# Kernel tuning notes

Measured on AMD Instinct MI355X. Metric: run time of the kernel, lower is better.

The kernel has to match this reference:

```python
import jax, jax.numpy as jnp
import numpy as np

D_STATE = 16
D_CONV = 4


def _ln_cf(x, w, b, eps=1e-6):
    # channels_first LayerNorm over dim 1 of (B,C,H,W)
    u = x.mean(1, keepdims=True)
    s = ((x - u) ** 2).mean(1, keepdims=True)
    return w[:, None, None] * ((x - u) / jnp.sqrt(s + eps)) + b[:, None, None]


def _ln_last(x, w, b, eps=1e-5):
    u = x.mean(-1, keepdims=True)
    s = ((x - u) ** 2).mean(-1, keepdims=True)
    return (x - u) / jnp.sqrt(s + eps) * w + b


def _mamba(xn, Win, convw, convb, Wx, Wdt, bdt, Alog, Dp):
    # xn: (B, L, d_model); returns (B, L, d_inner) (out_proj is Identity in this module)
    B, L, _ = xn.shape
    di = Win.shape[0] // 2
    xz = xn @ Win.T                                   # (B,L,2*di), in_proj bias=False
    xc, z = xz[..., :di], xz[..., di:]
    # causal depthwise conv1d along L (pad left d_conv-1, slice == torch pad+trim)
    xt = jnp.pad(xc.transpose(0, 2, 1), ((0, 0), (0, 0), (D_CONV - 1, 0)))
    xt = jax.lax.conv_general_dilated(xt, convw[:, None, :], (1,), 'VALID',
                                      dimension_numbers=('NCH', 'OIH', 'NCH'),
                                      feature_group_count=di)
    xs = jax.nn.silu(xt + convb[None, :, None]).transpose(0, 2, 1)  # (B,L,di)
    dtr = Wdt.shape[1]
    x_dbl = xs @ Wx.T                                 # (B,L,dtr+2*ds)
    dt = x_dbl[..., :dtr]
    Bm = x_dbl[..., dtr:dtr + D_STATE]                # (B,L,ds)
    Cm = x_dbl[..., dtr + D_STATE:]                   # (B,L,ds)
    delta = jax.nn.softplus(dt @ Wdt.T + bdt)         # (B,L,di)
    A = -jnp.exp(Alog)                                # (di,ds)
    dA = jnp.exp(delta[..., None] * A)                # (B,L,di,ds)
    dBx = delta[..., None] * Bm[:, :, None, :] * xs[..., None]

    def step(h, ab):
        a, b2 = ab
        h = a * h + b2
        return h, h

    h0 = jnp.zeros((B, di, D_STATE), xn.dtype)
    _, hs = jax.lax.scan(step, h0, (dA.transpose(1, 0, 2, 3), dBx.transpose(1, 0, 2, 3)))
    y = jnp.einsum('lbds,bls->bld', hs, Cm) + xs * Dp
    return y * jax.nn.silu(z)


def _dwconv2d(u, k, dil):
    c = k.shape[0]
    return jax.lax.conv_general_dilated(u, k[:, None], (1, 1),
                                        [(dil, dil), (dil, dil)],
                                        rhs_dilation=(dil, dil),
                                        dimension_numbers=('NCHW', 'OIHW', 'NCHW'),
                                        feature_group_count=c)


def _block(x, gamma1, gamma2, ln1_w, ln1_b, mn_w, mn_b,
           f_Win, f_convw, f_convb, f_Wx, f_Wdt, f_bdt, f_Alog, f_D,
           b_Win, b_convw, b_convb, b_Wx, b_Wdt, b_bdt, b_Alog, b_D,
           Wout, msff_win, msff_dw1, msff_dw2, msff_dw3, msff_wout):
    B, C, H, W = x.shape
    L = H * W
    # --- BiPixelMambaLayer branch ---
    x1 = _ln_cf(x, ln1_w, ln1_b)                       # norm1 (channels_first)
    xf = x1.reshape(B, C, L).transpose(0, 2, 1)        # (B,L,C)
    xn = _ln_last(xf, mn_w, mn_b)                      # inner nn.LayerNorm (eps=1e-5)
    yf = _mamba(xn, f_Win, f_convw, f_convb, f_Wx, f_Wdt, f_bdt, f_Alog, f_D)
    yb = _mamba(xn[:, ::-1], b_Win, b_convw, b_convb, b_Wx, b_Wdt, b_bdt, b_Alog, b_D)
    yo = (yf + yb[:, ::-1]) @ Wout.T                   # shared out_proj (bias=False)
    x = x + gamma1[:, None, None] * (yo.transpose(0, 2, 1).reshape(B, C, H, W) + x1)
    # --- MSFF branch (norm1 reused) ---
    inp = x
    xm = _ln_cf(x, ln1_w, ln1_b)
    h = jnp.einsum('oc,bchw->bohw', msff_win, xm)      # project_in (1x1x1 conv, depth=1)
    hid = msff_dw1.shape[0]
    h1 = _dwconv2d(h[:, :hid], msff_dw1, 1)            # Conv3d 3x3x3 w/ depth=1 == 2D center slice
    h2 = _dwconv2d(h[:, hid:2 * hid], msff_dw2, 2)
    h3 = _dwconv2d(h[:, 2 * hid:], msff_dw3, 3)
    g = jax.nn.gelu(h1, approximate=False) * h2 * h3
    xm = jnp.einsum('oc,bchw->bohw', msff_wout, g)     # project_out
    return inp + gamma2[:, None, None] * xm


def setup_inputs() -> dict:
    key = jax.random.key(0)
    ks = jax.random.split(key, 40)
    dim, di, dtr, ds, hid, Bn, H, W = 96, 192, 6, 16, 192, 2, 64, 64
    r = lambda i, shape, s=0.05: jax.random.normal(ks[i], shape, jnp.float32) * s
    inp = {
        'x': r(0, (Bn, dim, H, W), 1.0),
        'gamma1': r(1, (dim,), 0.1), 'gamma2': r(2, (dim,), 0.1),
        'ln1_w': 1.0 + r(3, (dim,), 0.1), 'ln1_b': r(4, (dim,), 0.1),
        'mn_w': 1.0 + r(5, (dim,), 0.1), 'mn_b': r(6, (dim,), 0.1),
    }
    i = 7
    for p in ('f_', 'b_'):
        inp[p + 'Win'] = r(i, (2 * di, dim)); i += 1
        inp[p + 'convw'] = r(i, (di, D_CONV), 0.2); i += 1
        inp[p + 'convb'] = r(i, (di,), 0.1); i += 1
        inp[p + 'Wx'] = r(i, (dtr + 2 * ds, di)); i += 1
        inp[p + 'Wdt'] = r(i, (di, dtr), 0.1); i += 1
        inp[p + 'bdt'] = r(i, (di,), 0.1); i += 1
        inp[p + 'Alog'] = jax.random.uniform(ks[i], (di, ds), jnp.float32, 0.0, 2.5); i += 1
        inp[p + 'D'] = r(i, (di,), 0.5); i += 1
    inp['Wout'] = r(i, (dim, di)); i += 1
    inp['msff_win'] = r(i, (3 * hid, dim)); i += 1
    inp['msff_dw1'] = r(i, (hid, 3, 3), 0.2); i += 1
    inp['msff_dw2'] = r(i, (hid, 3, 3), 0.2); i += 1
    inp['msff_dw3'] = r(i, (hid, 3, 3), 0.2); i += 1
    inp['msff_wout'] = r(i, (dim, hid)); i += 1
    return inp


def reference(x, gamma1, gamma2, ln1_w, ln1_b, mn_w, mn_b,
              f_Win, f_convw, f_convb, f_Wx, f_Wdt, f_bdt, f_Alog, f_D,
              b_Win, b_convw, b_convb, b_Wx, b_Wdt, b_bdt, b_Alog, b_D,
              Wout, msff_win, msff_dw1, msff_dw2, msff_dw3, msff_wout):
    return _block(x, gamma1, gamma2, ln1_w, ln1_b, mn_w, mn_b,
                  f_Win, f_convw, f_convb, f_Wx, f_Wdt, f_bdt, f_Alog, f_D,
                  b_Win, b_convw, b_convb, b_Wx, b_Wdt, b_bdt, b_Alog, b_D,
                  Wout, msff_win, msff_dw1, msff_dw2, msff_dw3, msff_wout)
```

## Files before the change

### kernel.cpp

```cpp
#include <hip/hip_runtime.h>
#include <hip/hip_bf16.h>
#include <math.h>

typedef __hip_bfloat16 bf16;
typedef _Float16 f16;
typedef f16  f16x8  __attribute__((ext_vector_type(8)));
typedef short short8 __attribute__((ext_vector_type(8)));
typedef unsigned short ushort8 __attribute__((ext_vector_type(8)));
typedef float floatx4 __attribute__((ext_vector_type(4)));

#define L_SEQ 4096
#define BATCH 2
#define DIM   96
#define DI    192
#define DS    16
#define HID   192
#define NPOS  (BATCH * L_SEQ)
#define NCH   1024
#define CHUNK 4
#define GRP   32
#define NGRP  (NCH / GRP)
#define NREC  (2 * BATCH * DI)
#define LDBL  40
#define LOG2E 1.44269504088896f
#define TP    32

__device__ __forceinline__ float silu_f(float x) { return x / (1.f + __expf(-x)); }
__device__ __forceinline__ float softplus_f(float x) {
    return fmaxf(x, 0.f) + __logf(1.f + __expf(-fabsf(x)));
}
__device__ __forceinline__ float b2f(bf16 v) { return __bfloat162float(v); }
__device__ __forceinline__ float us2f(unsigned short u) {
    union { unsigned int i; float f; } cv; cv.i = ((unsigned int)u) << 16; return cv.f;
}

__global__ void k_prep(const float* __restrict__ fWin, const float* __restrict__ bWin,
                       const float* __restrict__ fWx,  const float* __restrict__ bWx,
                       const float* __restrict__ Wout, const float* __restrict__ mwin,
                       const float* __restrict__ mwout,
                       const float* __restrict__ fAlog, const float* __restrict__ bAlog,
                       const float* __restrict__ mdw1, const float* __restrict__ mdw2,
                       const float* __restrict__ mdw3,
                       bf16* __restrict__ war, float* __restrict__ a2tab,
                       float* __restrict__ mdwt) {
    int i = blockIdx.x * blockDim.x + threadIdx.x;
    if (i < 180480) {
        float v;
        if (i < 36864)        v = fWin[i];
        else if (i < 73728)   v = bWin[i - 36864];
        else if (i < 81024)   v = fWx[i - 73728];
        else if (i < 88320)   v = bWx[i - 81024];
        else if (i < 106752)  v = Wout[i - 88320];
        else if (i < 162048)  v = mwin[i - 106752];
        else                  v = mwout[i - 162048];
        war[i] = __float2bfloat16(v);
    } else if (i < 186624) {
        int j = i - 180480;
        int dir = j / 3072, rem = j % 3072;
        const float* al = dir ? bAlog : fAlog;
        a2tab[j] = -__expf(al[rem]) * LOG2E;
    } else if (i < 191808) {
        int j = i - 186624;
        int cv = j / 1728, rem = j % 1728;
        int tap = rem / 192, c = rem % 192;
        const float* src = (cv == 0) ? mdw1 : (cv == 1) ? mdw2 : mdw3;
        mdwt[j] = src[c * 9 + tap];
    }
}

__global__ void k_ln12_t(const float* __restrict__ x,
                         const float* __restrict__ ln1w, const float* __restrict__ ln1b,
                         const float* __restrict__ mnw,  const float* __restrict__ mnb,
                         float* __restrict__ X1, bf16* __restrict__ XNbf) {
    __shared__ float xt[DIM][TP + 1];
    __shared__ float rs[8][TP], rss[8][TP];
    __shared__ float uu[TP], rr[TP];
    int p0 = blockIdx.x * TP;
    int b = p0 >> 12, l0 = p0 & (L_SEQ - 1);
    int t = threadIdx.x;
    int tg = t >> 5, li = t & 31;

    for (int idx = t; idx < DIM * TP; idx += 256) {
        int c = idx >> 5, q = idx & 31;
        xt[c][q] = x[((size_t)(b * DIM + c)) * L_SEQ + l0 + q];
    }
    __syncthreads();
    {
        float s = 0.f, ss = 0.f;
        for (int c = tg; c < DIM; c += 8) { float v = xt[c][li]; s += v; ss += v * v; }
        rs[tg][li] = s; rss[tg][li] = ss;
    }
    __syncthreads();
    if (t < TP) {
        float s = 0.f, ss = 0.f;
#pragma unroll
        for (int g = 0; g < 8; g++) { s += rs[g][t]; ss += rss[g][t]; }
        float u = s / DIM;
        uu[t] = u; rr[t] = rsqrtf(ss / DIM - u * u + 1e-6f);
    }
    __syncthreads();
    {
        float u = uu[li], r = rr[li];
        float s2 = 0.f, ss2 = 0.f;
        for (int c = tg; c < DIM; c += 8) {
            float tv = ln1w[c] * (xt[c][li] - u) * r + ln1b[c];
            X1[((size_t)(b * DIM + c)) * L_SEQ + l0 + li] = tv;
            xt[c][li] = tv;
            s2 += tv; ss2 += tv * tv;
        }
        rs[tg][li] = s2; rss[tg][li] = ss2;
    }
    __syncthreads();
    if (t < TP) {
        float s = 0.f, ss = 0.f;
#pragma unroll
        for (int g = 0; g < 8; g++) { s += rs[g][t]; ss += rss[g][t]; }
        float u = s / DIM;
        uu[t] = u; rr[t] = rsqrtf(ss / DIM - u * u + 1e-5f);
    }
    __syncthreads();
    for (int idx = t; idx < DIM * TP; idx += 256) {
        int q = idx / DIM, c = idx % DIM;
        XNbf[(size_t)(p0 + q) * DIM + c] =
            __float2bfloat16((xt[c][q] - uu[q]) * rr[q] * mnw[c] + mnb[c]);
    }
}

__global__ void mfma_nt_dir(const bf16* __restrict__ A0, const bf16* __restrict__ A1,
                            const bf16* __restrict__ W0, const bf16* __restrict__ W1,
                            void* __restrict__ C0, void* __restrict__ C1,
                            int M, int N, int K, int ldc, int pad6, int obf) {
    int z = blockIdx.z;
    const bf16* A = z ? A1 : A0;
    const bf16* W = z ? W1 : W0;
    void* C = z ? C1 : C0;
    int wave = threadIdx.x >> 6, lane = threadIdx.x & 63;
    int m0 = blockIdx.x * 64 + wave * 16;
    int n0 = blockIdx.y * 64;
    int lm = lane & 15, quad = lane >> 4;
    const short* Ap = (const short*)A + (size_t)(m0 + lm) * K + quad * 8;
    const short* Wp = (const short*)W;
    floatx4 acc[4];
#pragma unroll
    for (int t = 0; t < 4; t++) acc[t] = (floatx4){0.f, 0.f, 0.f, 0.f};
    for (int k0 = 0; k0 < K; k0 += 32) {
        short8 a = *(const short8*)(Ap + k0);
#pragma unroll
        for (int t = 0; t < 4; t++) {
            int n = n0 + t * 16 + lm;
            short8 b = (n < N) ? *(const short8*)(Wp + (size_t)n * K + k0 + quad * 8)
                               : (short8){0,0,0,0,0,0,0,0};
            acc[t] = __builtin_amdgcn_mfma_f32_16x16x32_bf16(a, b, acc[t], 0, 0, 0);
        }
    }
#pragma unroll
    for (int t = 0; t < 4; t++) {
        int n = n0 + t * 16 + lm;
        if (n < N) {
            int nn = (pad6 && n >= 6) ? n + 2 : n;
#pragma unroll
            for (int r = 0; r < 4; r++) {
                int m = m0 + quad * 4 + r;
                if (obf) ((bf16*)C)[(size_t)m * ldc + nn] = __float2bfloat16(acc[t][r]);
                else     ((float*)C)[(size_t)m * ldc + nn] = acc[t][r];
            }
        }
    }
}

__global__ void mfma_nt(const bf16* __restrict__ A, const bf16* __restrict__ W,
                        bf16* __restrict__ C, int M, int N, int K, int ldc) {
    int wave = threadIdx.x >> 6, lane = threadIdx.x & 63;
    int m0 = blockIdx.x * 64 + wave * 16;
    int n0 = blockIdx.y * 64;
    int lm = lane & 15, quad = lane >> 4;
    const short* Ap = (const short*)A + (size_t)(m0 + lm) * K + quad * 8;
    const short* Wp = (const short*)W;
    floatx4 acc[4];
#pragma unroll
    for (int t = 0; t < 4; t++) acc[t] = (floatx4){0.f, 0.f, 0.f, 0.f};
    for (int k0 = 0; k0 < K; k0 += 32) {
        short8 a = *(const short8*)(Ap + k0);
#pragma unroll
        for (int t = 0; t < 4; t++) {
            int n = n0 + t * 16 + lm;
            short8 b = (n < N) ? *(const short8*)(Wp + (size_t)n * K + k0 + quad * 8)
                               : (short8){0,0,0,0,0,0,0,0};
            acc[t] = __builtin_amdgcn_mfma_f32_16x16x32_bf16(a, b, acc[t], 0, 0, 0);
        }
    }
#pragma unroll
    for (int t = 0; t < 4; t++) {
        int n = n0 + t * 16 + lm;
        if (n < N) {
#pragma unroll
            for (int r = 0; r < 4; r++) {
                int m = m0 + quad * 4 + r;
                C[(size_t)m * ldc + n] = __float2bfloat16(acc[t][r]);
            }
        }
    }
}

__global__ void mfma_out(const bf16* __restrict__ Y1, const bf16* __restrict__ Y2,
                         const bf16* __restrict__ W, float* __restrict__ C,
                         int M, int N, int K, int ldc) {
    int wave = threadIdx.x >> 6, lane = threadIdx.x & 63;
    int m0 = blockIdx.x * 64 + wave * 16;
    int n0 = blockIdx.y * 64;
    int lm = lane & 15, quad = lane >> 4;
    const short* A1p = (const short*)Y1 + (size_t)(m0 + lm) * K + quad * 8;
    const short* A2p = (const short*)Y2 + (size_t)(m0 + lm) * K + quad * 8;
    const short* Wp  = (const short*)W;
    floatx4 acc[4];
#pragma unroll
    for (int t = 0; t < 4; t++) acc[t] = (floatx4){0.f, 0.f, 0.f, 0.f};
    for (int k0 = 0; k0 < K; k0 += 32) {
        short8 a1 = *(const short8*)(A1p + k0);
        short8 a2 = *(const short8*)(A2p + k0);
#pragma unroll
        for (int t = 0; t < 4; t++) {
            int n = n0 + t * 16 + lm;
            short8 b = (n < N) ? *(const short8*)(Wp + (size_t)n * K + k0 + quad * 8)
                               : (short8){0,0,0,0,0,0,0,0};
            acc[t] = __builtin_amdgcn_mfma_f32_16x16x32_bf16(a1, b, acc[t], 0, 0, 0);
            acc[t] = __builtin_amdgcn_mfma_f32_16x16x32_bf16(a2, b, acc[t], 0, 0, 0);
        }
    }
#pragma unroll
    for (int t = 0; t < 4; t++) {
        int n = n0 + t * 16 + lm;
        if (n < N) {
#pragma unroll
            for (int r = 0; r < 4; r++) {
                int m = m0 + quad * 4 + r;
                C[(size_t)m * ldc + n] = acc[t][r];
            }
        }
    }
}

__global__ void mfma_msffout(const bf16* __restrict__ A, const bf16* __restrict__ Bm,
                             const float* __restrict__ XMID, const float* __restrict__ gamma2,
                             float* __restrict__ out, int M, int K) {
    int wave = threadIdx.x >> 6, lane = threadIdx.x & 63;
    int m0 = blockIdx.x * 64 + wave * 16;
    int n0 = blockIdx.y * 64;
    int lm = lane & 15, quad = lane >> 4;
    int am = m0 + lm;
    bool aval = am < M;
    const short* Ap = (const short*)A + (size_t)am * K + quad * 8;
    const short* Bp = (const short*)Bm;
    floatx4 acc[4];
#pragma unroll
    for (int t = 0; t < 4; t++) acc[t] = (floatx4){0.f, 0.f, 0.f, 0.f};
    for (int k0 = 0; k0 < K; k0 += 32) {
        short8 a = aval ? *(const short8*)(Ap + k0) : (short8){0,0,0,0,0,0,0,0};
#pragma unroll
        for (int t = 0; t < 4; t++) {
            int n = n0 + t * 16 + lm;
            short8 b = *(const short8*)(Bp + (size_t)n * K + k0 + quad * 8);
            acc[t] = __builtin_amdgcn_mfma_f32_16x16x32_bf16(a, b, acc[t], 0, 0, 0);
        }
    }
#pragma unroll
    for (int t = 0; t < 4; t++) {
        int n = n0 + t * 16 + lm;
        int b = n >> 12, l = n & (L_SEQ - 1);
#pragma unroll
        for (int r = 0; r < 4; r++) {
            int m = m0 + quad * 4 + r;
            if (m < M) {
                size_t idx = ((size_t)(b * M + m)) * L_SEQ + l;
                out[idx] = XMID[idx] + gamma2[m] * acc[t][r];
            }
        }
    }
}

__global__ void k_conv_v(const bf16* __restrict__ XZF, const bf16* __restrict__ XZB,
                         const float* __restrict__ fw, const float* __restrict__ fb,
                         const float* __restrict__ bw, const float* __restrict__ bb,
                         bf16* __restrict__ XSF, bf16* __restrict__ XSB) {
    int dirb = blockIdx.y;
    int i = blockIdx.x * blockDim.x + threadIdx.x;
    int dg = i % 24;
    int p = i / 24;
    int b = p >> 12, l = p & (L_SEQ - 1);
    int d0 = dg * 8;
    const bf16* XZ = dirb ? XZB : XZF;
    const float* cw = dirb ? bw : fw;
    const float* cb = dirb ? bb : fb;

    float4 w[8];
#pragma unroll
    for (int j = 0; j < 8; j++) w[j] = *(const float4*)(cw + (d0 + j) * 4);
    float acc[8];
#pragma unroll
    for (int j = 0; j < 8; j++) acc[j] = cb[d0 + j];

#pragma unroll
    for (int k = 0; k < 4; k++) {
        int ls = dirb ? (l + 3 - k) : (l - 3 + k);
        if (ls >= 0 && ls < L_SEQ) {
            ushort8 xv = *(const ushort8*)((const unsigned short*)XZ +
                           ((size_t)(b * L_SEQ + ls)) * 384 + d0);
#pragma unroll
            for (int j = 0; j < 8; j++) {
                float wk = (k == 0) ? w[j].x : (k == 1) ? w[j].y : (k == 2) ? w[j].z : w[j].w;
                acc[j] += wk * us2f(xv[j]);
            }
        }
    }
    ushort8 ov;
#pragma unroll
    for (int j = 0; j < 8; j++) {
        bf16 t = __float2bfloat16(silu_f(acc[j]));
        ov[j] = *(unsigned short*)&t;
    }
    *(ushort8*)((unsigned short*)(dirb ? XSB : XSF) + (size_t)p * DI + d0) = ov;
}

__global__ void k_scan_p1(const float* __restrict__ DBLF, const float* __restrict__ DBLB,
                          const bf16* __restrict__ XSF,  const bf16* __restrict__ XSB,
                          const float* __restrict__ fWdt, const float* __restrict__ fbdt,
                          const float* __restrict__ bWdt, const float* __restrict__ bbdt,
                          const float* __restrict__ a2tab,
                          f16* __restrict__ P, f16* __restrict__ Q) {
    int t = blockIdx.x * blockDim.x + threadIdx.x;
    int d = t % DI;
    int g = t / DI;
    int chunk = g & (NCH - 1);
    int dirb = g >> 10;
    int b = dirb & 1, dir = dirb >> 1;

    const float* DBL = dir ? DBLB : DBLF;
    const bf16*  XS  = dir ? XSB  : XSF;
    const float* wdt = (dir ? bWdt : fWdt) + d * 6;
    float bdtv = (dir ? bbdt : fbdt)[d];

    float wd[6];
#pragma unroll
    for (int r = 0; r < 6; r++) wd[r] = wdt[r];
    const float* a2p = a2tab + (dir * DI + d) * 16;
    float A2[16], h[16];
#pragma unroll
    for (int v = 0; v < 4; v++) {
        float4 a2v = *(const float4*)(a2p + 4 * v);
        A2[4*v] = a2v.x; A2[4*v+1] = a2v.y; A2[4*v+2] = a2v.z; A2[4*v+3] = a2v.w;
    }
#pragma unroll
    for (int s = 0; s < 16; s++) h[s] = 0.f;

    int l = dir ? (L_SEQ - 1 - chunk * CHUNK) : chunk * CHUNK;
    int stp = dir ? -1 : 1;
    float sumdel = 0.f;

#pragma unroll
    for (int i = 0; i < CHUNK; i++) {
        size_t p = (size_t)b * L_SEQ + l;
        const float* row = DBL + p * LDBL;
        float dtv = bdtv;
#pragma unroll
        for (int r = 0; r < 6; r++) dtv += row[r] * wd[r];
        float del = softplus_f(dtv);
        float xs  = b2f(XS[p * DI + d]);
        const float4* bm = (const float4*)(row + 8);
        float4 B0 = bm[0], B1 = bm[1], B2 = bm[2], B3 = bm[3];
        float Bm[16] = {B0.x,B0.y,B0.z,B0.w, B1.x,B1.y,B1.z,B1.w,
                        B2.x,B2.y,B2.z,B2.w, B3.x,B3.y,B3.z,B3.w};
        float dx = del * xs;
        sumdel += del;
#pragma unroll
        for (int s = 0; s < 16; s++) {
            float dA = exp2f(del * A2[s]);
            h[s] = dA * h[s] + dx * Bm[s];
        }
        l += stp;
    }
    size_t idx = ((size_t)g * DI + d) * 16;
    f16x8 q0, q1, p0, p1;
#pragma unroll
    for (int j = 0; j < 8; j++) {
        q0[j] = (f16)h[j];
        q1[j] = (f16)h[8 + j];
        p0[j] = (f16)exp2f(A2[j] * sumdel);
        p1[j] = (f16)exp2f(A2[8 + j] * sumdel);
    }
    *(f16x8*)(Q + idx)     = q0;
    *(f16x8*)(Q + idx + 8) = q1;
    *(f16x8*)(P + idx)     = p0;
    *(f16x8*)(P + idx + 8) = p1;
}

__global__ void k_scan_p2a(const f16* __restrict__ P, const f16* __restrict__ Q,
                           float* __restrict__ Pg, float* __restrict__ Qg) {
    int t = blockIdx.x * blockDim.x + threadIdx.x;
    int s8 = t & 1;
    int d = (t >> 1) % DI;
    int rest = t / (DI * 2);
    int grp = rest % NGRP;
    int dirb = rest / NGRP;

    float Pr[8], Qr[8];
#pragma unroll
    for (int j = 0; j < 8; j++) { Pr[j] = 1.f; Qr[j] = 0.f; }

    size_t base = (((size_t)(dirb * NCH + grp * GRP)) * DI + d) * 16 + s8 * 8;
    for (int i = 0; i < GRP; i++) {
        size_t idx = base + (size_t)i * (DI * 16);
        f16x8 p8 = *(const f16x8*)(P + idx);
        f16x8 q8 = *(const f16x8*)(Q + idx);
#pragma unroll
        for (int j = 0; j < 8; j++) {
            float pv = (float)p8[j], qv = (float)q8[j];
            Qr[j] = pv * Qr[j] + qv;
            Pr[j] *= pv;
        }
    }
    size_t gidx = (((size_t)(dirb * NGRP + grp)) * DI + d) * 16 + s8 * 8;
#pragma unroll
    for (int v = 0; v < 2; v++) {
        *(float4*)(Pg + gidx + 4 * v) = make_float4(Pr[4*v], Pr[4*v+1], Pr[4*v+2], Pr[4*v+3]);
        *(float4*)(Qg + gidx + 4 * v) = make_float4(Qr[4*v], Qr[4*v+1], Qr[4*v+2], Qr[4*v+3]);
    }
}

__global__ void k_scan_p2b(const float* __restrict__ Pg, float* __restrict__ Qg) {
    int u = blockIdx.x * blockDim.x + threadIdx.x;
    int s = u & 15;
    int dd = (u >> 4) % DI;
    int dirb = u / (DI * 16);
    float runP = 1.f, runQ = 0.f;
#pragma unroll
    for (int g = 0; g < NGRP; g++) {
        size_t i = (((size_t)(dirb * NGRP + g)) * DI + dd) * 16 + s;
        float pg = Pg[i], qg = Qg[i];
        Qg[i] = runQ;
        runQ = pg * runQ + qg;
        runP *= pg;
    }
}

__global__ void k_scan_p2c(const f16* __restrict__ P, f16* __restrict__ Q,
                           const float* __restrict__ Qg) {
    int t = blockIdx.x * blockDim.x + threadIdx.x;
    int s8 = t & 1;
    int d = (t >> 1) % DI;
    int rest = t / (DI * 2);
    int grp = rest % NGRP;
    int dirb = rest / NGRP;

    size_t gidx = (((size_t)(dirb * NGRP + grp)) * DI + d) * 16 + s8 * 8;
    float runQ[8];
#pragma unroll
    for (int v = 0; v < 2; v++) {
        float4 qv = *(const float4*)(Qg + gidx + 4 * v);
        runQ[4*v] = qv.x; runQ[4*v+1] = qv.y; runQ[4*v+2] = qv.z; runQ[4*v+3] = qv.w;
    }

    size_t base = (((size_t)(dirb * NCH + grp * GRP)) * DI + d) * 16 + s8 * 8;
    for (int i = 0; i < GRP; i++) {
        size_t idx = base + (size_t)i * (DI * 16);
        f16x8 p8 = *(const f16x8*)(P + idx);
        f16x8 q8 = *(const f16x8*)(Q + idx);
        f16x8 o8;
#pragma unroll
        for (int j = 0; j < 8; j++) {
            o8[j] = (f16)runQ[j];
            runQ[j] = (float)p8[j] * runQ[j] + (float)q8[j];
        }
        *(f16x8*)(Q + idx) = o8;
    }
}

__global__ void k_scan_p3(const float* __restrict__ DBLF, const float* __restrict__ DBLB,
                          const bf16* __restrict__ XSF,  const bf16* __restrict__ XSB,
                          const bf16* __restrict__ XZF,  const bf16* __restrict__ XZB,
                          const float* __restrict__ fWdt, const float* __restrict__ fbdt,
                          const float* __restrict__ bWdt, const float* __restrict__ bbdt,
                          const float* __restrict__ a2tab,
                          const float* __restrict__ fD,    const float* __restrict__ bD,
                          const f16* __restrict__ Q,
                          bf16* __restrict__ YSF, bf16* __restrict__ YSB) {
    int t = blockIdx.x * blockDim.x + threadIdx.x;
    int d = t % DI;
    int g = t / DI;
    int chunk = g & (NCH - 1);
    int dirb = g >> 10;
    int b = dirb & 1, dir = dirb >> 1;

    const float* DBL = dir ? DBLB : DBLF;
    const bf16*  XS  = dir ? XSB  : XSF;
    const bf16*  XZ  = dir ? XZB  : XZF;
    const float* wdt = (dir ? bWdt : fWdt) + d * 6;
    float bdtv = (dir ? bbdt : fbdt)[d];
    float Dp = dir ? bD[d] : fD[d];
    bf16* Y = dir ? YSB : YSF;

    float wd[6];
#pragma unroll
    for (int r = 0; r < 6; r++) wd[r] = wdt[r];
    const float* a2p = a2tab + (dir * DI + d) * 16;
    float A2[16], h[16];
#pragma unroll
    for (int v = 0; v < 4; v++) {
        float4 a2v = *(const float4*)(a2p + 4 * v);
        A2[4*v] = a2v.x; A2[4*v+1] = a2v.y; A2[4*v+2] = a2v.z; A2[4*v+3] = a2v.w;
    }
    size_t idx = ((size_t)g * DI + d) * 16;
    f16x8 q0 = *(const f16x8*)(Q + idx);
    f16x8 q1 = *(const f16x8*)(Q + idx + 8);
#pragma unroll
    for (int j = 0; j < 8; j++) { h[j] = (float)q0[j]; h[8 + j] = (float)q1[j]; }

    int l = dir ? (L_SEQ - 1 - chunk * CHUNK) : chunk * CHUNK;
    int stp = dir ? -1 : 1;

#pragma unroll
    for (int i = 0; i < CHUNK; i++) {
        size_t p = (size_t)b * L_SEQ + l;
        const float* row = DBL + p * LDBL;
        float dtv = bdtv;
#pragma unroll
        for (int r = 0; r < 6; r++) dtv += row[r] * wd[r];
        float del = softplus_f(dtv);
        float xs  = b2f(XS[p * DI + d]);
        float z   = b2f(XZ[p * 384 + 192 + d]);
        const float4* bm = (const float4*)(row + 8);
        float4 B0 = bm[0], B1 = bm[1], B2 = bm[2], B3 = bm[3];
        float4 C0 = bm[4], C1 = bm[5], C2 = bm[6], C3 = bm[7];
        float Bm[16] = {B0.x,B0.y,B0.z,B0.w, B1.x,B1.y,B1.z,B1.w,
                        B2.x,B2.y,B2.z,B2.w, B3.x,B3.y,B3.z,B3.w};
        float Cm[16] = {C0.x,C0.y,C0.z,C0.w, C1.x,C1.y,C1.z,C1.w,
                        C2.x,C2.y,C2.z,C2.w, C3.x,C3.y,C3.z,C3.w};
        float dx = del * xs;
        float pr = 0.f;
#pragma unroll
        for (int s = 0; s < 16; s++) {
            float dA = exp2f(del * A2[s]);
            h[s] = dA * h[s] + dx * Bm[s];
            pr += h[s] * Cm[s];
        }
        Y[p * DI + d] = __float2bfloat16((pr + xs * Dp) * silu_f(z));
        l += stp;
    }
}

__global__ void k_mid_t(const float* __restrict__ x, const float* __restrict__ YO,
                        const float* __restrict__ X1,
                        const float* __restrict__ gamma1,
                        const float* __restrict__ ln1w, const float* __restrict__ ln1b,
                        float* __restrict__ XMID, bf16* __restrict__ XM2cl) {
    __shared__ float vt[DIM][TP + 1];
    __shared__ float yt[DIM][TP + 1];
    __shared__ float rs[8][TP], rss[8][TP];
    __shared__ float uu[TP], rr[TP];
    int p0 = blockIdx.x * TP;
    int b = p0 >> 12, l0 = p0 & (L_SEQ - 1);
    int t = threadIdx.x;
    int tg = t >> 5, li = t & 31;

    for (int idx = t; idx < DIM * TP; idx += 256) {
        int q = idx / DIM, c = idx % DIM;
        yt[c][q] = YO[(size_t)(p0 + q) * DIM + c];
    }
    __syncthreads();
    {
        float s = 0.f, ss = 0.f;
        for (int c = tg; c < DIM; c += 8) {
            size_t gi = ((size_t)(b * DIM + c)) * L_SEQ + l0 + li;
            float v = x[gi] + gamma1[c] * (yt[c][li] + X1[gi]);
            XMID[gi] = v;
            vt[c][li] = v;
            s += v; ss += v * v;
        }
        rs[tg][li] = s; rss[tg][li] = ss;
    }
    __syncthreads();
    if (t < TP) {
        float s = 0.f, ss = 0.f;
#pragma unroll
        for (int g = 0; g < 8; g++) { s += rs[g][t]; ss += rss[g][t]; }
        float u = s / DIM;
        uu[t] = u; rr[t] = rsqrtf(ss / DIM - u * u + 1e-6f);
    }
    __syncthreads();
    for (int idx = t; idx < DIM * TP; idx += 256) {
        int q = idx / DIM, c = idx % DIM;
        XM2cl[(size_t)(p0 + q) * DIM + c] =
            __float2bfloat16(ln1w[c] * (vt[c][q] - uu[q]) * rr[q] + ln1b[c]);
    }
}

__global__ void k_msff_v(const bf16* __restrict__ H, const float* __restrict__ mdwt,
                         bf16* __restrict__ G) {
    int i = blockIdx.x * blockDim.x + threadIdx.x;
    int cg = i % 24;
    int p = i / 24;
    int c0 = cg * 8;
    int b = p >> 12, l = p & (L_SEQ - 1);
    int y = l >> 6, xc = l & 63;
    float a1[8] = {}, a2[8] = {}, a3[8] = {};
    const unsigned short* Hu = (const unsigned short*)H;

#pragma unroll
    for (int ky = 0; ky < 3; ky++) {
#pragma unroll
        for (int kx = 0; kx < 3; kx++) {
            int tap = ky * 3 + kx;
            {
                int y1 = y + (ky - 1), x1 = xc + (kx - 1);
                if (y1 >= 0 && y1 < 64 && x1 >= 0 && x1 < 64) {
                    float4 w0 = *(const float4*)(mdwt + tap * 192 + c0);
                    float4 w1 = *(const float4*)(mdwt + tap * 192 + c0 + 4);
                    ushort8 hv = *(const ushort8*)(Hu +
                        ((size_t)(b * L_SEQ + y1 * 64 + x1)) * 576 + c0);
                    float wv[8] = {w0.x,w0.y,w0.z,w0.w, w1.x,w1.y,w1.z,w1.w};
#pragma unroll
                    for (int j = 0; j < 8; j++) a1[j] += wv[j] * us2f(hv[j]);
                }
            }
            {
                int y2 = y + (ky - 1) * 2, x2 = xc + (kx - 1) * 2;
                if (y2 >= 0 && y2 < 64 && x2 >= 0 && x2 < 64) {
                    float4 w0 = *(const float4*)(mdwt + (9 + tap) * 192 + c0);
                    float4 w1 = *(const float4*)(mdwt + (9 + tap) * 192 + c0 + 4);
                    ushort8 hv = *(const ushort8*)(Hu +
                        ((size_t)(b * L_SEQ + y2 * 64 + x2)) * 576 + 192 + c0);
                    float wv[8] = {w0.x,w0.y,w0.z,w0.w, w1.x,w1.y,w1.z,w1.w};
#pragma unroll
                    for (int j = 0; j < 8; j++) a2[j] += wv[j] * us2f(hv[j]);
                }
            }
            {
                int y3 = y + (ky - 1) * 3, x3 = xc + (kx - 1) * 3;
                if (y3 >= 0 && y3 < 64 && x3 >= 0 && x3 < 64) {
                    float4 w0 = *(const float4*)(mdwt + (18 + tap) * 192 + c0);
                    float4 w1 = *(const float4*)(mdwt + (18 + tap) * 192 + c0 + 4);
                    ushort8 hv = *(const ushort8*)(Hu +
                        ((size_t)(b * L_SEQ + y3 * 64 + x3)) * 576 + 384 + c0);
                    float wv[8] = {w0.x,w0.y,w0.z,w0.w, w1.x,w1.y,w1.z,w1.w};
#pragma unroll
                    for (int j = 0; j < 8; j++) a3[j] += wv[j] * us2f(hv[j]);
                }
            }
        }
    }
    ushort8 ov;
#pragma unroll
    for (int j = 0; j < 8; j++) {
        float ge = 0.5f * a1[j] * (1.f + erff(a1[j] * 0.70710678118f));
        bf16 t = __float2bfloat16(ge * a2[j] * a3[j]);
        ov[j] = *(unsigned short*)&t;
    }
    *(ushort8*)((unsigned short*)G + (size_t)p * HID + c0) = ov;
}

extern "C" void kernel_launch(void* const* d_in, const int* in_sizes, int n_in,
                              void* d_out, int out_size, void* d_ws, size_t ws_size,
                              hipStream_t stream) {
    const float* x      = (const float*)d_in[0];
    const float* gamma1 = (const float*)d_in[1];
    const float* gamma2 = (const float*)d_in[2];
    const float* ln1w   = (const float*)d_in[3];
    const float* ln1b   = (const float*)d_in[4];
    const float* mnw    = (const float*)d_in[5];
    const float* mnb    = (const float*)d_in[6];
    const float* fWin   = (const float*)d_in[7];
    const float* fconvw = (const float*)d_in[8];
    const float* fconvb = (const float*)d_in[9];
    const float* fWx    = (const float*)d_in[10];
    const float* fWdt   = (const float*)d_in[11];
    const float* fbdt   = (const float*)d_in[12];
    const float* fAlog  = (const float*)d_in[13];
    const float* fD     = (const float*)d_in[14];
    const float* bWin   = (const float*)d_in[15];
    const float* bconvw = (const float*)d_in[16];
    const float* bconvb = (const float*)d_in[17];
    const float* bWx    = (const float*)d_in[18];
    const float* bWdt   = (const float*)d_in[19];
    const float* bbdt   = (const float*)d_in[20];
    const float* bAlog  = (const float*)d_in[21];
    const float* bD     = (const float*)d_in[22];
    const float* Wout   = (const float*)d_in[23];
    const float* mwin   = (const float*)d_in[24];
    const float* mdw1   = (const float*)d_in[25];
    const float* mdw2   = (const float*)d_in[26];
    const float* mdw3   = (const float*)d_in[27];
    const float* mwout  = (const float*)d_in[28];
    float* out = (float*)d_out;

    float* ws = (float*)d_ws;
    float* X1    = ws;
    bf16*  XNbf  = (bf16*)(ws + 786432);
    bf16*  XZF   = (bf16*)(ws + 1179648);
    bf16*  XZB   = (bf16*)(ws + 2752512);
    bf16*  XSF   = (bf16*)(ws + 4325376);
    bf16*  XSB   = (bf16*)(ws + 5111808);
    float* DBLF  = ws + 5898240;
    float* DBLB  = ws + 6225920;
    f16*   Ph    = (f16*)(ws + 6553600);
    f16*   Qh    = (f16*)(ws + 12845056);
    bf16*  YSFbf = (bf16*)(ws + 19136512);
    bf16*  YSBbf = (bf16*)(ws + 19922944);
    float* YO    = ws + 20709376;
    float* XMID  = ws + 21495808;
    bf16*  XM2cl = (bf16*)(ws + 22282240);
    bf16*  Hcl   = (bf16*)(ws + 22675456);
    bf16*  Gcl   = (bf16*)(ws + 25034752);
    bf16*  WAR   = (bf16*)(ws + 25821184);
    float* A2tab = ws + 25911424;
    float* MDWT  = ws + 25917568;
    float* Pgb   = ws + 25922752;
    float* Qgb   = ws + 26315968;

    const bf16* fWinB  = WAR;
    const bf16* bWinB  = WAR + 36864;
    const bf16* fWxB   = WAR + 73728;
    const bf16* bWxB   = WAR + 81024;
    const bf16* WoutB  = WAR + 88320;
    const bf16* mwinB  = WAR + 106752;
    const bf16* mwoutB = WAR + 162048;

    k_prep<<<750, 256, 0, stream>>>(fWin, bWin, fWx, bWx, Wout, mwin, mwout,
                                    fAlog, bAlog, mdw1, mdw2, mdw3,
                                    WAR, A2tab, MDWT);
    k_ln12_t<<<NPOS / TP, 256, 0, stream>>>(x, ln1w, ln1b, mnw, mnb, X1, XNbf);
    mfma_nt_dir<<<dim3(128, 6, 2), 256, 0, stream>>>(XNbf, XNbf, fWinB, bWinB,
                                                     XZF, XZB, NPOS, 384, DIM, 384, 0, 1);
    k_conv_v<<<dim3(NPOS * 24 / 256, 2), 256, 0, stream>>>(XZF, XZB, fconvw, fconvb,
                                                           bconvw, bconvb, XSF, XSB);
    mfma_nt_dir<<<dim3(128, 1, 2), 256, 0, stream>>>(XSF, XSB, fWxB, bWxB,
                                                     DBLF, DBLB, NPOS, 38, DI, LDBL, 1, 0);
    k_scan_p1<<<NREC * NCH / 256, 256, 0, stream>>>(DBLF, DBLB, XSF, XSB,
                                                    fWdt, fbdt, bWdt, bbdt,
                                                    A2tab, Ph, Qh);
    k_scan_p2a<<<4 * NGRP * DI * 2 / 256, 256, 0, stream>>>(Ph, Qh, Pgb, Qgb);
    k_scan_p2b<<<NREC * 16 / 256, 256, 0, stream>>>(Pgb, Qgb);
    k_scan_p2c<<<4 * NGRP * DI * 2 / 256, 256, 0, stream>>>(Ph, Qh, Qgb);
    k_scan_p3<<<NREC * NCH / 256, 256, 0, stream>>>(DBLF, DBLB, XSF, XSB, XZF, XZB,
                                                    fWdt, fbdt, bWdt, bbdt,
                                                    A2tab, fD, bD, Qh,
                                                    YSFbf, YSBbf);
    mfma_out<<<dim3(128, 2), 256, 0, stream>>>(YSFbf, YSBbf, WoutB, YO, NPOS, DIM, DI, DIM);
    k_mid_t<<<NPOS / TP, 256, 0, stream>>>(x, YO, X1, gamma1, ln1w, ln1b, XMID, XM2cl);
    mfma_nt<<<dim3(128, 9), 256, 0, stream>>>(XM2cl, mwinB, Hcl, NPOS, 576, DIM, 576);
    k_msff_v<<<NPOS * 24 / 256, 256, 0, stream>>>(Hcl, MDWT, Gcl);
    mfma_msffout<<<dim3(2, 128), 256, 0, stream>>>(mwoutB, Gcl, XMID, gamma2, out, DIM, HID);
}
```

Before: 290.0 us.

## Recompute LN1 in mid kernel and halve scan chunk count

The LN1 output X1 is no longer written to global memory by the first layernorm kernel. The mid kernel now reloads x and recomputes LN1 statistics in shared memory instead of reading X1, which removes a full fp32 activation write and read at the cost of an extra reduction pass. The chunked scan also moves from 1024 chunks of 4 steps to 512 chunks of 8 steps, which halves the P/Q intermediate traffic and the group-combine work but lowers parallelism in the scan passes. The inner scan loops are no longer force-unrolled, and an unused running product in the group pass is dropped.

```diff
diff --git a/kernel.cpp b/kernel.cpp
--- a/kernel.cpp
+++ b/kernel.cpp
@@ -16,8 +16,8 @@
 #define DS    16
 #define HID   192
 #define NPOS  (BATCH * L_SEQ)
-#define NCH   1024
-#define CHUNK 4
+#define NCH   512
+#define CHUNK 8
 #define GRP   32
 #define NGRP  (NCH / GRP)
 #define NREC  (2 * BATCH * DI)
@@ -71,7 +71,7 @@
 __global__ void k_ln12_t(const float* __restrict__ x,
                          const float* __restrict__ ln1w, const float* __restrict__ ln1b,
                          const float* __restrict__ mnw,  const float* __restrict__ mnb,
-                         float* __restrict__ X1, bf16* __restrict__ XNbf) {
+                         bf16* __restrict__ XNbf) {
     __shared__ float xt[DIM][TP + 1];
     __shared__ float rs[8][TP], rss[8][TP];
     __shared__ float uu[TP], rr[TP];
@@ -104,7 +104,6 @@
         float s2 = 0.f, ss2 = 0.f;
         for (int c = tg; c < DIM; c += 8) {
             float tv = ln1w[c] * (xt[c][li] - u) * r + ln1b[c];
-            X1[((size_t)(b * DIM + c)) * L_SEQ + l0 + li] = tv;
             xt[c][li] = tv;
             s2 += tv; ss2 += tv * tv;
         }
@@ -331,7 +330,7 @@
     int d = t % DI;
     int g = t / DI;
     int chunk = g & (NCH - 1);
-    int dirb = g >> 10;
+    int dirb = g >> 9;
     int b = dirb & 1, dir = dirb >> 1;
 
     const float* DBL = dir ? DBLB : DBLF;
@@ -356,7 +355,6 @@
     int stp = dir ? -1 : 1;
     float sumdel = 0.f;
 
-#pragma unroll
     for (int i = 0; i < CHUNK; i++) {
         size_t p = (size_t)b * L_SEQ + l;
         const float* row = DBL + p * LDBL;
@@ -431,14 +429,13 @@
     int s = u & 15;
     int dd = (u >> 4) % DI;
     int dirb = u / (DI * 16);
-    float runP = 1.f, runQ = 0.f;
+    float runQ = 0.f;
 #pragma unroll
     for (int g = 0; g < NGRP; g++) {
         size_t i = (((size_t)(dirb * NGRP + g)) * DI + dd) * 16 + s;
         float pg = Pg[i], qg = Qg[i];
         Qg[i] = runQ;
         runQ = pg * runQ + qg;
-        runP *= pg;
     }
 }
 
@@ -487,7 +484,7 @@
     int d = t % DI;
     int g = t / DI;
     int chunk = g & (NCH - 1);
-    int dirb = g >> 10;
+    int dirb = g >> 9;
     int b = dirb & 1, dir = dirb >> 1;
 
     const float* DBL = dir ? DBLB : DBLF;
@@ -517,7 +514,6 @@
     int l = dir ? (L_SEQ - 1 - chunk * CHUNK) : chunk * CHUNK;
     int stp = dir ? -1 : 1;
 
-#pragma unroll
     for (int i = 0; i < CHUNK; i++) {
         size_t p = (size_t)b * L_SEQ + l;
         const float* row = DBL + p * LDBL;
@@ -548,11 +544,10 @@
 }
 
 __global__ void k_mid_t(const float* __restrict__ x, const float* __restrict__ YO,
-                        const float* __restrict__ X1,
                         const float* __restrict__ gamma1,
                         const float* __restrict__ ln1w, const float* __restrict__ ln1b,
                         float* __restrict__ XMID, bf16* __restrict__ XM2cl) {
-    __shared__ float vt[DIM][TP + 1];
+    __shared__ float xt[DIM][TP + 1];
     __shared__ float yt[DIM][TP + 1];
     __shared__ float rs[8][TP], rss[8][TP];
     __shared__ float uu[TP], rr[TP];
@@ -562,19 +557,17 @@
     int tg = t >> 5, li = t & 31;
 
     for (int idx = t; idx < DIM * TP; idx += 256) {
+        int c = idx >> 5, q = idx & 31;
+        xt[c][q] = x[((size_t)(b * DIM + c)) * L_SEQ + l0 + q];
+    }
+    for (int idx = t; idx < DIM * TP; idx += 256) {
         int q = idx / DIM, c = idx % DIM;
         yt[c][q] = YO[(size_t)(p0 + q) * DIM + c];
     }
     __syncthreads();
     {
         float s = 0.f, ss = 0.f;
-        for (int c = tg; c < DIM; c += 8) {
-            size_t gi = ((size_t)(b * DIM + c)) * L_SEQ + l0 + li;
-            float v = x[gi] + gamma1[c] * (yt[c][li] + X1[gi]);
-            XMID[gi] = v;
-            vt[c][li] = v;
-            s += v; ss += v * v;
-        }
+        for (int c = tg; c < DIM; c += 8) { float v = xt[c][li]; s += v; ss += v * v; }
         rs[tg][li] = s; rss[tg][li] = ss;
     }
     __syncthreads();
@@ -586,10 +579,32 @@
         uu[t] = u; rr[t] = rsqrtf(ss / DIM - u * u + 1e-6f);
     }
     __syncthreads();
+    {
+        float u = uu[li], r = rr[li];
+        float s = 0.f, ss = 0.f;
+        for (int c = tg; c < DIM; c += 8) {
+            float xv = xt[c][li];
+            float x1 = ln1w[c] * (xv - u) * r + ln1b[c];
+            float v = xv + gamma1[c] * (yt[c][li] + x1);
+            XMID[((size_t)(b * DIM + c)) * L_SEQ + l0 + li] = v;
+            xt[c][li] = v;
+            s += v; ss += v * v;
+        }
+        rs[tg][li] = s; rss[tg][li] = ss;
+    }
+    __syncthreads();
+    if (t < TP) {
+        float s = 0.f, ss = 0.f;
+#pragma unroll
+        for (int g = 0; g < 8; g++) { s += rs[g][t]; ss += rss[g][t]; }
+        float u = s / DIM;
+        uu[t] = u; rr[t] = rsqrtf(ss / DIM - u * u + 1e-6f);
+    }
+    __syncthreads();
     for (int idx = t; idx < DIM * TP; idx += 256) {
         int q = idx / DIM, c = idx % DIM;
         XM2cl[(size_t)(p0 + q) * DIM + c] =
-            __float2bfloat16(ln1w[c] * (vt[c][q] - uu[q]) * rr[q] + ln1b[c]);
+            __float2bfloat16(ln1w[c] * (xt[c][q] - uu[q]) * rr[q] + ln1b[c]);
     }
 }
 
@@ -692,28 +707,27 @@
     float* out = (float*)d_out;
 
     float* ws = (float*)d_ws;
-    float* X1    = ws;
-    bf16*  XNbf  = (bf16*)(ws + 786432);
-    bf16*  XZF   = (bf16*)(ws + 1179648);
-    bf16*  XZB   = (bf16*)(ws + 2752512);
-    bf16*  XSF   = (bf16*)(ws + 4325376);
-    bf16*  XSB   = (bf16*)(ws + 5111808);
-    float* DBLF  = ws + 5898240;
-    float* DBLB  = ws + 6225920;
-    f16*   Ph    = (f16*)(ws + 6553600);
-    f16*   Qh    = (f16*)(ws + 12845056);
-    bf16*  YSFbf = (bf16*)(ws + 19136512);
-    bf16*  YSBbf = (bf16*)(ws + 19922944);
-    float* YO    = ws + 20709376;
-    float* XMID  = ws + 21495808;
-    bf16*  XM2cl = (bf16*)(ws + 22282240);
-    bf16*  Hcl   = (bf16*)(ws + 22675456);
-    bf16*  Gcl   = (bf16*)(ws + 25034752);
-    bf16*  WAR   = (bf16*)(ws + 25821184);
-    float* A2tab = ws + 25911424;
-    float* MDWT  = ws + 25917568;
-    float* Pgb   = ws + 25922752;
-    float* Qgb   = ws + 26315968;
+    bf16*  XNbf  = (bf16*)(ws);
+    bf16*  XZF   = (bf16*)(ws + 393216);
+    bf16*  XZB   = (bf16*)(ws + 1966080);
+    bf16*  XSF   = (bf16*)(ws + 3538944);
+    bf16*  XSB   = (bf16*)(ws + 4325376);
+    float* DBLF  = ws + 5111808;
+    float* DBLB  = ws + 5439488;
+    f16*   Ph    = (f16*)(ws + 5767168);
+    f16*   Qh    = (f16*)(ws + 8912896);
+    bf16*  YSFbf = (bf16*)(ws + 12058624);
+    bf16*  YSBbf = (bf16*)(ws + 12845056);
+    float* YO    = ws + 13631488;
+    float* XMID  = ws + 14417920;
+    bf16*  XM2cl = (bf16*)(ws + 15204352);
+    bf16*  Hcl   = (bf16*)(ws + 15597568);
+    bf16*  Gcl   = (bf16*)(ws + 17956864);
+    bf16*  WAR   = (bf16*)(ws + 18743296);
+    float* A2tab = ws + 18833536;
+    float* MDWT  = ws + 18839680;
+    float* Pgb   = ws + 18844864;
+    float* Qgb   = ws + 19041472;
 
     const bf16* fWinB  = WAR;
     const bf16* bWinB  = WAR + 36864;
@@ -726,7 +740,7 @@
     k_prep<<<750, 256, 0, stream>>>(fWin, bWin, fWx, bWx, Wout, mwin, mwout,
                                     fAlog, bAlog, mdw1, mdw2, mdw3,
                                     WAR, A2tab, MDWT);
-    k_ln12_t<<<NPOS / TP, 256, 0, stream>>>(x, ln1w, ln1b, mnw, mnb, X1, XNbf);
+    k_ln12_t<<<NPOS / TP, 256, 0, stream>>>(x, ln1w, ln1b, mnw, mnb, XNbf);
     mfma_nt_dir<<<dim3(128, 6, 2), 256, 0, stream>>>(XNbf, XNbf, fWinB, bWinB,
                                                      XZF, XZB, NPOS, 384, DIM, 384, 0, 1);
     k_conv_v<<<dim3(NPOS * 24 / 256, 2), 256, 0, stream>>>(XZF, XZB, fconvw, fconvb,
@@ -744,7 +758,7 @@
                                                     A2tab, fD, bD, Qh,
                                                     YSFbf, YSBbf);
     mfma_out<<<dim3(128, 2), 256, 0, stream>>>(YSFbf, YSBbf, WoutB, YO, NPOS, DIM, DI, DIM);
-    k_mid_t<<<NPOS / TP, 256, 0, stream>>>(x, YO, X1, gamma1, ln1w, ln1b, XMID, XM2cl);
+    k_mid_t<<<NPOS / TP, 256, 0, stream>>>(x, YO, gamma1, ln1w, ln1b, XMID, XM2cl);
     mfma_nt<<<dim3(128, 9), 256, 0, stream>>>(XM2cl, mwinB, Hcl, NPOS, 576, DIM, 576);
     k_msff_v<<<NPOS * 24 / 256, 256, 0, stream>>>(Hcl, MDWT, Gcl);
     mfma_msffout<<<dim3(2, 128), 256, 0, stream>>>(mwoutB, Gcl, XMID, gamma2, out, DIM, HID);
```

Result: no change. 288.3 us, median of 2 (-0.6%).
